# Optimization experiments

Measured on AMD Instinct MI355X. Metric: run time of the kernel, lower is better.

## Reference

```python
import jax, jax.numpy as jnp
import numpy as np

N_POINTS = 2_097_152  # ~1448x1448 sample points
N_CELLS = 5
N_SHAPES = 3 * N_CELLS * N_CELLS  # 75 primitives (tri, circle, ellipse per cell)


def _build_params():
    # Replicates the structure of VectorGraphicsRGB2IntegrandSlang.__init__:
    # per cell: triangle (11 floats), circle (8 floats), ellipse (9 floats).
    rng = np.random.default_rng(42)
    n, jf = N_CELLS, 1.0
    cw = 1.0 / n
    params = []
    for i in range(n):
        for j in range(n):
            bx = (i + 0.5) / n + (rng.random() - 0.5) * jf * cw
            by = (j + 0.5) / n + (rng.random() - 0.5) * jf * cw
            rad = 0.4 / n
            ang = np.sort(rng.random(3) * 2.0 * 3.14159)
            pxs = np.clip(bx + rad * np.cos(ang), 0.0, 1.0)
            pys = np.clip(by + rad * np.sin(ang), 0.0, 1.0)
            params += [1.0, pxs[0], pys[0], pxs[1], pys[1], pxs[2], pys[2], 0.0] + list(rng.random(3))
            cxx = (i + 0.5) / n + (rng.random() - 0.5) * jf * cw
            cyy = (j + 0.5) / n + (rng.random() - 0.5) * jf * cw
            cr = rng.random() * 0.1 / n + 0.05 / n
            cxx = min(max(cxx, cr), 1.0 - cr)
            cyy = min(max(cyy, cr), 1.0 - cr)
            params += [3.0, cxx, cyy, cr, 0.0] + list(rng.random(3))
            exx = (i + 0.5) / n + (rng.random() - 0.5) * jf * cw
            eyy = (j + 0.5) / n + (rng.random() - 0.5) * jf * cw
            erx = rng.random() * 0.12 / n + 0.04 / n
            ery = rng.random() * 0.12 / n + 0.04 / n
            exx = min(max(exx, erx), 1.0 - erx)
            eyy = min(max(eyy, ery), 1.0 - ery)
            params += [2.0, exx, eyy, erx, ery, 0.0] + list(rng.random(3))
    return np.asarray(params, dtype=np.float32)  # [700]


def setup_inputs() -> dict:
    key = jax.random.key(0)
    k1, _ = jax.random.split(key)
    x = jax.random.uniform(k1, (N_POINTS, 2), dtype=jnp.float32)  # points in [0,1]^2
    p = jnp.asarray(_build_params())
    return {"x": x, "p": p}


def reference(x, p):
    # Parse the fixed-layout parameter vector: 25 cells x 28 floats.
    cells = p.reshape(N_CELLS * N_CELLS, 28)
    tri, circ, ell = cells[:, :11], cells[:, 11:19], cells[:, 19:]
    px, py = x[:, 0:1], x[:, 1:2]  # [N,1] broadcast against [25] shapes

    # Triangle containment: consistent sign of the three edge cross products.
    ax, ay, bx, by, cx, cy = (tri[:, k] for k in range(1, 7))
    e0 = (px - ax) * (by - ay) - (py - ay) * (bx - ax)  # [N,25]
    e1 = (px - bx) * (cy - by) - (py - by) * (cx - bx)
    e2 = (px - cx) * (ay - cy) - (py - cy) * (ax - cx)
    tri_in = ((e0 >= 0) & (e1 >= 0) & (e2 >= 0)) | ((e0 <= 0) & (e1 <= 0) & (e2 <= 0))

    # Circle containment.
    ocx, ocy, orr = circ[:, 1], circ[:, 2], circ[:, 3]
    circ_in = (px - ocx) ** 2 + (py - ocy) ** 2 <= orr ** 2

    # Ellipse containment.
    ecx, ecy, erx, ery = ell[:, 1], ell[:, 2], ell[:, 3], ell[:, 4]
    ell_in = ((px - ecx) / erx) ** 2 + ((py - ecy) / ery) ** 2 <= 1.0

    # Interleave per-cell in shader evaluation order: triangle, circle, ellipse.
    inside = jnp.stack([tri_in, circ_in, ell_in], axis=2).reshape(x.shape[0], N_SHAPES)
    colors = jnp.stack([tri[:, 8:11], circ[:, 5:8], ell[:, 6:9]], axis=1).reshape(N_SHAPES, 3)

    last = (N_SHAPES - 1) - jnp.argmax(inside[:, ::-1], axis=1)  # [N]
    any_in = inside.any(axis=1)
    return jnp.where(any_in[:, None], colors[last], jnp.zeros((), x.dtype))  # [N,3]
```

## Files before the change

kernel.cpp:

```cpp
#include <hip/hip_runtime.h>

#pragma clang fp contract(off)

#define NPTS 2097152
#define PPT  2
#define NTHREADS (NPTS / PPT)

#define L_B    196
#define L_C    392
#define L_D    588
#define L_COL  784
#define LDS_FLOATS (784 + 304)

#define EPS_E 1e-5f

__device__ __noinline__ int exact_point(float px, float py, int ih, int jh,
                                        const float* __restrict__ p) {
    int idx = -1;
#pragma clang loop unroll(disable)
    for (int s = 0; s < 4; ++s) {
        int ii = ih - 1 + (s >> 1), jj = jh - 1 + (s & 1);
        if ((unsigned)ii > 4u || (unsigned)jj > 4u) continue;
        int c = 5 * ii + jj;
        const float* cell = p + 28 * c;
        float ax = cell[1], ay = cell[2], bx = cell[3], by = cell[4], cx = cell[5], cy = cell[6];
        float e0 = (px - ax) * (by - ay) - (py - ay) * (bx - ax);
        float e1 = (px - bx) * (cy - by) - (py - by) * (cx - bx);
        float e2 = (px - cx) * (ay - cy) - (py - cy) * (ax - cx);
        bool tin = (e0 >= 0.f && e1 >= 0.f && e2 >= 0.f) ||
                   (e0 <= 0.f && e1 <= 0.f && e2 <= 0.f);
        if (tin) idx = 3 * c;
        float dx = px - cell[12], dy = py - cell[13];
        if (dx * dx + dy * dy <= cell[14] * cell[14]) idx = 3 * c + 1;
        float u = (px - cell[20]) / cell[22];
        float v = (py - cell[21]) / cell[23];
        if (u * u + v * v <= 1.0f) idx = 3 * c + 2;
    }
    return idx;
}

__global__ __launch_bounds__(256) void vg_fused(const float* __restrict__ x,
                                                const float* __restrict__ p,
                                                float* __restrict__ out) {
    __shared__ float lds[LDS_FLOATS];
    int tl = threadIdx.x;
    int t  = blockIdx.x * 256 + tl;

    if (tl < 49) {
        int gi = tl / 7, gj = tl % 7;
        float4* A = (float4*)lds;
        float4* B = (float4*)(lds + L_B);
        float4* C = (float4*)(lds + L_C);
        float4* D = (float4*)(lds + L_D);
        if (gi >= 1 && gi <= 5 && gj >= 1 && gj <= 5) {
            int c = (gi - 1) * 5 + (gj - 1);
            const float* cell = p + c * 28;
            A[tl] = make_float4(cell[1], cell[2], cell[3], cell[4]);
            B[tl] = make_float4(cell[5], cell[6], cell[12], cell[13]);
            C[tl] = make_float4(cell[14], cell[20], cell[21], 1.0f / cell[22]);
            D[tl] = make_float4(1.0f / cell[23], 0.f, 0.f, 0.f);
        } else {
            A[tl] = make_float4(0.f, -2.f, 1.f, -2.f);
            B[tl] = make_float4(0.f, -3.f, 50.f, 50.f);
            C[tl] = make_float4(0.f, 50.f, 50.f, 1.f);
            D[tl] = make_float4(1.f, 0.f, 0.f, 0.f);
        }
    }
    if (tl >= 128 && tl < 204) {
        int e = tl - 128;
        float* col = lds + L_COL + e * 4;
        if (e < 75) {
            int c = e / 3, kind = e - 3 * c;
            const float* cell = p + c * 28;
            int base = (kind == 0) ? 8 : (kind == 1) ? 16 : 25;
            col[0] = cell[base]; col[1] = cell[base + 1]; col[2] = cell[base + 2];
        } else {
            col[0] = 0.f; col[1] = 0.f; col[2] = 0.f;
        }
        col[3] = 0.f;
    }
    __syncthreads();

    float4 xv = ((const float4*)x)[t];
    float PX[PPT] = {xv.x, xv.z};
    float PY[PPT] = {xv.y, xv.w};
    int idx[PPT], ih[PPT], jh[PPT], sb[PPT], cb[PPT];
    bool unc[PPT];

#pragma unroll
    for (int k = 0; k < PPT; ++k) {
        ih[k] = (int)floorf(__builtin_fmaf(PX[k], 5.0f, 0.4025f));
        jh[k] = (int)floorf(__builtin_fmaf(PY[k], 5.0f, 0.4025f));
        cb[k] = 7 * ih[k] + jh[k];
        sb[k] = 15 * ih[k] + 3 * jh[k] - 18;
        idx[k] = -1; unc[k] = false;
    }

    const float4* LA = (const float4*)lds;
    const float4* LB = (const float4*)(lds + L_B);
    const float4* LC = (const float4*)(lds + L_C);
    const int coff[4] = {0, 1, 7, 8};
    const int soff[4] = {0, 3, 15, 18};

#pragma unroll
    for (int k = 0; k < PPT; ++k) {
        float X = PX[k], Y = PY[k];
#pragma unroll
        for (int s = 0; s < 4; ++s) {
            int ci = cb[k] + coff[s];
            float4 A = LA[ci];
            float4 B = LB[ci];
            float4 C = LC[ci];
            float iry = lds[L_D + 4 * ci];
            int sid = sb[k] + soff[s];

            float d0y = A.w - A.y, d0x = A.z - A.x;
            float d1y = B.y - A.w, d1x = B.x - A.z;
            float d2y = A.y - B.y, d2x = A.x - B.x;
            float e0 = (X - A.x) * d0y - (Y - A.y) * d0x;
            float e1 = (X - A.z) * d1y - (Y - A.w) * d1x;
            float e2 = (X - B.x) * d2y - (Y - B.y) * d2x;
            bool tin = (e0 >= 0.f && e1 >= 0.f && e2 >= 0.f) ||
                       (e0 <= 0.f && e1 <= 0.f && e2 <= 0.f);
            idx[k] = tin ? sid : idx[k];

            float r2 = C.x * C.x;
            float dx = X - B.z, dy = Y - B.w;
            float tc = dx * dx + dy * dy;
            idx[k] = (tc <= r2) ? sid + 1 : idx[k];

            float ex = X - C.y, ey = Y - C.z;
            float u = ex * C.w, v = ey * iry;
            float te = __builtin_fmaf(u, u, v * v);
            unc[k] = unc[k] | (__builtin_fabsf(te - 1.0f) < EPS_E);
            idx[k] = (te <= 1.0f) ? sid + 2 : idx[k];
        }
    }

#pragma unroll
    for (int k = 0; k < PPT; ++k)
        if (__builtin_expect(unc[k], 0))
            idx[k] = exact_point(PX[k], PY[k], ih[k], jh[k], p);

    const float4* col4 = (const float4*)(lds + L_COL);
    float4 c0 = col4[idx[0] < 0 ? 75 : idx[0]];
    float4 c1 = col4[idx[1] < 0 ? 75 : idx[1]];

    float2* o2 = (float2*)out;
    o2[3 * t + 0] = make_float2(c0.x, c0.y);
    o2[3 * t + 1] = make_float2(c0.z, c1.x);
    o2[3 * t + 2] = make_float2(c1.y, c1.z);
}

extern "C" void kernel_launch(void* const* d_in, const int* in_sizes, int n_in,
                              void* d_out, int out_size, void* d_ws, size_t ws_size,
                              hipStream_t stream) {
    const float* x = (const float*)d_in[0];
    const float* p = (const float*)d_in[1];
    float* out = (float*)d_out;
    (void)d_ws; (void)ws_size;

    vg_fused<<<NTHREADS / 256, 256, 0, stream>>>(x, p, out);
}
```

Before: 79.33 us.

## Process four chunks per block and fetch colors from global instead of LDS

Each block now loops over four consecutive 256-thread chunks, so the per-block LDS setup of the shape table and its barrier are amortized over four times as many points, and the grid is a quarter of the size. The color table staging in LDS is removed. Colors are instead read straight from the parameter array in global memory, which should be cache-resident, at the cost of an integer divide and a scattered global load per point. The fewer, longer blocks may reduce latency hiding for the streaming loads and stores.

```diff
diff --git a/kernel.cpp b/kernel.cpp
--- a/kernel.cpp
+++ b/kernel.cpp
@@ -5,12 +5,13 @@
 #define NPTS 2097152
 #define PPT  2
 #define NTHREADS (NPTS / PPT)
+#define CHUNKS 4
+#define NBLOCKS (NTHREADS / 256 / CHUNKS)
 
 #define L_B    196
 #define L_C    392
 #define L_D    588
-#define L_COL  784
-#define LDS_FLOATS (784 + 304)
+#define LDS_FLOATS 784
 
 #define EPS_E 1e-5f
 
@@ -44,7 +45,6 @@
                                                 float* __restrict__ out) {
     __shared__ float lds[LDS_FLOATS];
     int tl = threadIdx.x;
-    int t  = blockIdx.x * 256 + tl;
 
     if (tl < 49) {
         int gi = tl / 7, gj = tl % 7;
@@ -66,35 +66,7 @@
             D[tl] = make_float4(1.f, 0.f, 0.f, 0.f);
         }
     }
-    if (tl >= 128 && tl < 204) {
-        int e = tl - 128;
-        float* col = lds + L_COL + e * 4;
-        if (e < 75) {
-            int c = e / 3, kind = e - 3 * c;
-            const float* cell = p + c * 28;
-            int base = (kind == 0) ? 8 : (kind == 1) ? 16 : 25;
-            col[0] = cell[base]; col[1] = cell[base + 1]; col[2] = cell[base + 2];
-        } else {
-            col[0] = 0.f; col[1] = 0.f; col[2] = 0.f;
-        }
-        col[3] = 0.f;
-    }
     __syncthreads();
-
-    float4 xv = ((const float4*)x)[t];
-    float PX[PPT] = {xv.x, xv.z};
-    float PY[PPT] = {xv.y, xv.w};
-    int idx[PPT], ih[PPT], jh[PPT], sb[PPT], cb[PPT];
-    bool unc[PPT];
-
-#pragma unroll
-    for (int k = 0; k < PPT; ++k) {
-        ih[k] = (int)floorf(__builtin_fmaf(PX[k], 5.0f, 0.4025f));
-        jh[k] = (int)floorf(__builtin_fmaf(PY[k], 5.0f, 0.4025f));
-        cb[k] = 7 * ih[k] + jh[k];
-        sb[k] = 15 * ih[k] + 3 * jh[k] - 18;
-        idx[k] = -1; unc[k] = false;
-    }
 
     const float4* LA = (const float4*)lds;
     const float4* LB = (const float4*)(lds + L_B);
@@ -102,54 +74,83 @@
     const int coff[4] = {0, 1, 7, 8};
     const int soff[4] = {0, 3, 15, 18};
 
-#pragma unroll
-    for (int k = 0; k < PPT; ++k) {
-        float X = PX[k], Y = PY[k];
-#pragma unroll
-        for (int s = 0; s < 4; ++s) {
-            int ci = cb[k] + coff[s];
-            float4 A = LA[ci];
-            float4 B = LB[ci];
-            float4 C = LC[ci];
-            float iry = lds[L_D + 4 * ci];
-            int sid = sb[k] + soff[s];
+#pragma unroll 1
+    for (int it = 0; it < CHUNKS; ++it) {
+        int t = (blockIdx.x * CHUNKS + it) * 256 + tl;
 
-            float d0y = A.w - A.y, d0x = A.z - A.x;
-            float d1y = B.y - A.w, d1x = B.x - A.z;
-            float d2y = A.y - B.y, d2x = A.x - B.x;
-            float e0 = (X - A.x) * d0y - (Y - A.y) * d0x;
-            float e1 = (X - A.z) * d1y - (Y - A.w) * d1x;
-            float e2 = (X - B.x) * d2y - (Y - B.y) * d2x;
-            bool tin = (e0 >= 0.f && e1 >= 0.f && e2 >= 0.f) ||
-                       (e0 <= 0.f && e1 <= 0.f && e2 <= 0.f);
-            idx[k] = tin ? sid : idx[k];
-
-            float r2 = C.x * C.x;
-            float dx = X - B.z, dy = Y - B.w;
-            float tc = dx * dx + dy * dy;
-            idx[k] = (tc <= r2) ? sid + 1 : idx[k];
-
-            float ex = X - C.y, ey = Y - C.z;
-            float u = ex * C.w, v = ey * iry;
-            float te = __builtin_fmaf(u, u, v * v);
-            unc[k] = unc[k] | (__builtin_fabsf(te - 1.0f) < EPS_E);
-            idx[k] = (te <= 1.0f) ? sid + 2 : idx[k];
-        }
-    }
+        float4 xv = ((const float4*)x)[t];
+        float PX[PPT] = {xv.x, xv.z};
+        float PY[PPT] = {xv.y, xv.w};
+        int idx[PPT], ih[PPT], jh[PPT], sb[PPT], cb[PPT];
+        bool unc[PPT];
 
 #pragma unroll
-    for (int k = 0; k < PPT; ++k)
-        if (__builtin_expect(unc[k], 0))
-            idx[k] = exact_point(PX[k], PY[k], ih[k], jh[k], p);
+        for (int k = 0; k < PPT; ++k) {
+            ih[k] = (int)floorf(__builtin_fmaf(PX[k], 5.0f, 0.4025f));
+            jh[k] = (int)floorf(__builtin_fmaf(PY[k], 5.0f, 0.4025f));
+            cb[k] = 7 * ih[k] + jh[k];
+            sb[k] = 15 * ih[k] + 3 * jh[k] - 18;
+            idx[k] = -1; unc[k] = false;
+        }
 
-    const float4* col4 = (const float4*)(lds + L_COL);
-    float4 c0 = col4[idx[0] < 0 ? 75 : idx[0]];
-    float4 c1 = col4[idx[1] < 0 ? 75 : idx[1]];
+#pragma unroll
+        for (int k = 0; k < PPT; ++k) {
+            float X = PX[k], Y = PY[k];
+#pragma unroll
+            for (int s = 0; s < 4; ++s) {
+                int ci = cb[k] + coff[s];
+                float4 A = LA[ci];
+                float4 B = LB[ci];
+                float4 C = LC[ci];
+                float iry = lds[L_D + 4 * ci];
+                int sid = sb[k] + soff[s];
 
-    float2* o2 = (float2*)out;
-    o2[3 * t + 0] = make_float2(c0.x, c0.y);
-    o2[3 * t + 1] = make_float2(c0.z, c1.x);
-    o2[3 * t + 2] = make_float2(c1.y, c1.z);
+                float d0y = A.w - A.y, d0x = A.z - A.x;
+                float d1y = B.y - A.w, d1x = B.x - A.z;
+                float d2y = A.y - B.y, d2x = A.x - B.x;
+                float e0 = (X - A.x) * d0y - (Y - A.y) * d0x;
+                float e1 = (X - A.z) * d1y - (Y - A.w) * d1x;
+                float e2 = (X - B.x) * d2y - (Y - B.y) * d2x;
+                bool tin = (e0 >= 0.f && e1 >= 0.f && e2 >= 0.f) ||
+                           (e0 <= 0.f && e1 <= 0.f && e2 <= 0.f);
+                idx[k] = tin ? sid : idx[k];
+
+                float r2 = C.x * C.x;
+                float dx = X - B.z, dy = Y - B.w;
+                float tc = dx * dx + dy * dy;
+                idx[k] = (tc <= r2) ? sid + 1 : idx[k];
+
+                float ex = X - C.y, ey = Y - C.z;
+                float u = ex * C.w, v = ey * iry;
+                float te = __builtin_fmaf(u, u, v * v);
+                unc[k] = unc[k] | (__builtin_fabsf(te - 1.0f) < EPS_E);
+                idx[k] = (te <= 1.0f) ? sid + 2 : idx[k];
+            }
+        }
+
+#pragma unroll
+        for (int k = 0; k < PPT; ++k)
+            if (__builtin_expect(unc[k], 0))
+                idx[k] = exact_point(PX[k], PY[k], ih[k], jh[k], p);
+
+        float col[PPT][3];
+#pragma unroll
+        for (int k = 0; k < PPT; ++k) {
+            int id = idx[k] < 0 ? 0 : idx[k];
+            int c = id / 3, kind = id - 3 * c;
+            int off = 28 * c + (kind == 0 ? 8 : (kind == 1 ? 16 : 25));
+            float r = p[off], g = p[off + 1], b = p[off + 2];
+            bool none = idx[k] < 0;
+            col[k][0] = none ? 0.f : r;
+            col[k][1] = none ? 0.f : g;
+            col[k][2] = none ? 0.f : b;
+        }
+
+        float2* o2 = (float2*)out;
+        o2[3 * t + 0] = make_float2(col[0][0], col[0][1]);
+        o2[3 * t + 1] = make_float2(col[0][2], col[1][0]);
+        o2[3 * t + 2] = make_float2(col[1][1], col[1][2]);
+    }
 }
 
 extern "C" void kernel_launch(void* const* d_in, const int* in_sizes, int n_in,
@@ -160,5 +161,5 @@
     float* out = (float*)d_out;
     (void)d_ws; (void)ws_size;
 
-    vg_fused<<<NTHREADS / 256, 256, 0, stream>>>(x, p, out);
+    vg_fused<<<NBLOCKS, 256, 0, stream>>>(x, p, out);
 }
```

Result: no change. 80.74 us (+1.8%).
